# Kernel optimization log

Measured on AMD Instinct MI355X. Metric: run time of the kernel, lower is better.

The kernel has to match this reference:

```python
import jax, jax.numpy as jnp
import numpy as np

B, S, LATENT = 256, 64, 20
U_DIM = LATENT // 5            # 4
T_HID, T_DEPTH = 20, 4         # treatment MLP
D_HID, D_DEPTH = 4 * LATENT, 4 # drift MLP (80 hidden)
T_LEN = 41
DT = 0.05
SIGMA, THETA, MU = 0.5, 1.0, 0.0
N = B * S
DIM_AUG = LATENT + 2           # latent + logqp + Tx


def _mlp(x, w_in, b_in, w_h, b_h, w_out, b_out, act):
    # input layer always ReLU (MLPSimple), hidden layers use `act`
    h = jax.nn.relu(x @ w_in.T + b_in)
    for i in range(w_h.shape[0]):
        h = act(h @ w_h[i].T + b_h[i])
    return h @ w_out.T + b_out


def setup_inputs() -> dict:
    key = jax.random.key(0)
    ks = jax.random.split(key, 20)

    def lin(k, out_d, in_d):
        bound = 1.0 / np.sqrt(in_d)
        return jax.random.uniform(k, (out_d, in_d), jnp.float32, -bound, bound)

    def bias(k, out_d, in_d):
        bound = 1.0 / np.sqrt(in_d)
        return jax.random.uniform(k, (out_d,), jnp.float32, -bound, bound)

    return {
        "z_SDE": jax.random.normal(ks[0], (B, S, LATENT), jnp.float32),
        "t": jnp.arange(T_LEN, dtype=jnp.float32) * DT,
        "Tx": jax.random.uniform(ks[1], (B,), jnp.float32),
        "noise": jax.random.normal(ks[2], (T_LEN - 1, N, DIM_AUG), jnp.float32),
        # treatment MLP: 1 -> 20 (ReLU) -> [20->20 ReLU]x4 -> 4
        "tw_in": lin(ks[3], T_HID, 1),
        "tb_in": bias(ks[4], T_HID, 1),
        "tw_h": jnp.stack([lin(jax.random.fold_in(ks[5], i), T_HID, T_HID) for i in range(T_DEPTH)]),
        "tb_h": jnp.stack([bias(jax.random.fold_in(ks[6], i), T_HID, T_HID) for i in range(T_DEPTH)]),
        "tw_out": lin(ks[7], U_DIM, T_HID),
        "tb_out": bias(ks[8], U_DIM, T_HID),
        # drift MLP: 24 -> 80 (ReLU) -> [80->80 Tanh]x4 -> 20
        "dw_in": lin(ks[9], D_HID, LATENT + U_DIM),
        "db_in": bias(ks[10], D_HID, LATENT + U_DIM),
        "dw_h": jnp.stack([lin(jax.random.fold_in(ks[11], i), D_HID, D_HID) for i in range(D_DEPTH)]),
        "db_h": jnp.stack([bias(jax.random.fold_in(ks[12], i), D_HID, D_HID) for i in range(D_DEPTH)]),
        "dw_out": lin(ks[13], LATENT, D_HID),
        "db_out": bias(ks[14], LATENT, D_HID),
    }


def reference(z_SDE, t, Tx, noise, tw_in, tb_in, tw_h, tb_h, tw_out, tb_out,
              dw_in, db_in, dw_h, db_h, dw_out, db_out):
    # build augmented initial state: [z, logqp0=0, Tx]  -> [N, DIM_AUG]
    Tx_rep = jnp.broadcast_to(Tx[:, None, None], (B, S, 1))
    aug_y0 = jnp.concatenate(
        [z_SDE, jnp.zeros((B, S, 1), z_SDE.dtype), Tx_rep.astype(z_SDE.dtype)], axis=-1
    ).reshape(N, DIM_AUG)

    dt = t[1] - t[0]           # 0.05, aligned with euler dt
    sqrt_dt = jnp.sqrt(dt)
    # diagonal diffusion: sigma on latent dims, 0 on (logqp, Tx) aug dims
    g_diag = jnp.concatenate([jnp.full((LATENT,), SIGMA, jnp.float32), jnp.zeros((2,), jnp.float32)])

    def f_aug(ti, y_aug):
        T_ = y_aug[:, -1]                     # treatment indicator
        y = y_aug[:, :LATENT]
        t_col = jnp.broadcast_to(ti, (N, 1)).astype(y.dtype)
        u = _mlp(t_col, tw_in, tb_in, tw_h, tb_h, tw_out, tb_out, jax.nn.relu)
        u_t = u * T_[:, None]
        h = THETA * (MU - y)                  # prior drift
        f = _mlp(jnp.concatenate([y, u_t], axis=-1), dw_in, db_in, dw_h, db_h, dw_out, db_out, jnp.tanh) - h
        # _stable_division(f - h, g); g = sigma = 0.5 > eps so plain division
        uu = (f - h) / SIGMA
        f_logqp = 0.5 * jnp.sum(uu * uu, axis=1, keepdims=True)
        return jnp.concatenate([f, f_logqp, jnp.zeros_like(f_logqp)], axis=1)

    def step(y, inp):
        ti, dW = inp
        y_new = y + f_aug(ti, y) * dt + g_diag[None, :] * (dW * sqrt_dt)
        return y_new, y_new

    _, ys_rest = jax.lax.scan(step, aug_y0, (t[:-1], noise))
    aug_ys = jnp.concatenate([aug_y0[None], ys_rest], axis=0)   # [T, N, DIM_AUG]
    # faithful to source: raw reshape of [T, N, dim] into [B, S, T, dim]
    aug_ys = aug_ys.reshape(-1, S, T_LEN, DIM_AUG)
    ys = aug_ys[:, :, :, :-2]
    logqp = aug_ys[:, :, -1, -2]
    return ys, logqp
```

## Files before the change

kernel.cpp:

```cpp
#include <hip/hip_runtime.h>
#include <math.h>
#include <stdint.h>

#define NPART 16384
#define NSTEP 40
#define DIMA  22
#define OUT0_ELEMS 13434880
#define TRAJ_OFF   160

typedef __attribute__((ext_vector_type(8))) short short8;
typedef __attribute__((ext_vector_type(4))) float floatx4;
typedef __attribute__((ext_vector_type(4))) int   intx4;

union V4 { intx4 i; short8 s; floatx4 f; };

__device__ __forceinline__ uint32_t bf16r(float x) {
    uint32_t u = __float_as_uint(x);
    u += 0x7FFFu + ((u >> 16) & 1u);
    return u >> 16;
}
__device__ __forceinline__ uint32_t pk2(float a0, float a1) {
    return bf16r(a0) | (bf16r(a1) << 16);
}
__device__ __forceinline__ float fast_tanh(float x) {
    float e = __expf(2.0f * x);
    return 1.0f - 2.0f * __builtin_amdgcn_rcpf(e + 1.0f);
}

__device__ __forceinline__ V4 load8(const float* p) {
    floatx4 v0 = *(const floatx4*)p;
    floatx4 v1 = *(const floatx4*)(p + 4);
    V4 r;
    r.i = (intx4){ (int)pk2(v0[0], v0[1]), (int)pk2(v0[2], v0[3]),
                   (int)pk2(v1[0], v1[1]), (int)pk2(v1[2], v1[3]) };
    return r;
}

#define BUILD_B3(B0, B1, B2, PK)                                               \
    {                                                                          \
        _Pragma("unroll")                                                      \
        for (int w = 0; w < 4; w++) {                                          \
            int s = (((w >> 1) + 2 * quad) & 3) * 16 + n15;                    \
            int a0 = __shfl((int)PK[0][w & 1], s);                             \
            int a1 = __shfl((int)PK[1][w & 1], s);                             \
            B0[w] = (quad >= 2) ? a1 : a0;                                     \
            int a2 = __shfl((int)PK[2][w & 1], s);                             \
            int a3 = __shfl((int)PK[3][w & 1], s);                             \
            B1[w] = (quad >= 2) ? a3 : a2;                                     \
            int a4 = __shfl((int)PK[4][w & 1], s);                             \
            B2[w] = (quad >= 2) ? 0 : a4;                                      \
        }                                                                      \
    }

__global__ __launch_bounds__(256, 1) void sde_mfma(
    const float* __restrict__ z,      const float* __restrict__ t_arr,
    const float* __restrict__ Tx,     const float* __restrict__ noise,
    const float* __restrict__ dw_in,  const float* __restrict__ db_in,
    const float* __restrict__ dw_h,   const float* __restrict__ db_h,
    const float* __restrict__ dw_out, const float* __restrict__ db_out,
    const float* __restrict__ tw_in,  const float* __restrict__ tb_in,
    const float* __restrict__ tw_h,   const float* __restrict__ tb_h,
    const float* __restrict__ tw_out, const float* __restrict__ tb_out,
    float* __restrict__ out0,         float* __restrict__ traj)
{
    __shared__ float sb[592];
    const int tid = threadIdx.x;

    for (int di = tid; di < 432; di += 256) {
        float v;
        if (di < 80)       v = db_in[di];
        else if (di < 400) v = db_h[di - 80];
        else               v = (di - 400 < 20) ? db_out[di - 400] : 0.f;
        sb[di] = v;
    }
    if (tid < NSTEP) {
        float ti = t_arr[tid];
        float hh[20], h2[20];
        #pragma unroll
        for (int j = 0; j < 20; j++) {
            float v = tw_in[j] * ti + tb_in[j];
            hh[j] = v > 0.f ? v : 0.f;
        }
        #pragma unroll
        for (int l = 0; l < 4; l++) {
            #pragma unroll
            for (int j = 0; j < 20; j++) {
                float a = tb_h[l * 20 + j];
                #pragma unroll
                for (int k = 0; k < 20; k++) a += tw_h[(l * 20 + j) * 20 + k] * hh[k];
                h2[j] = a > 0.f ? a : 0.f;
            }
            #pragma unroll
            for (int j = 0; j < 20; j++) hh[j] = h2[j];
        }
        #pragma unroll
        for (int c = 0; c < 4; c++) {
            float a = tb_out[c];
            #pragma unroll
            for (int k = 0; k < 20; k++) a += tw_out[c * 20 + k] * hh[k];
            sb[432 + tid * 4 + c] = a;
        }
    }

    const int lane = tid & 63;
    const int n15  = lane & 15;
    const int quad = lane >> 4;
    const int wv   = tid >> 6;
    const int n    = blockIdx.x * 64 + wv * 16 + n15;
    const float Txb = Tx[blockIdx.x];
    const float dtv = t_arr[1] - t_arr[0];
    const float sdt = sqrtf(dtv);
    const intx4 zero4 = {0, 0, 0, 0};

    V4 wAin[5], wAh[4][5][3], wAout[2][3];
    {
        #pragma unroll
        for (int mt = 0; mt < 5; mt++) {
            if (quad < 3) wAin[mt] = load8(dw_in + (mt * 16 + n15) * 24 + quad * 8);
            else          wAin[mt].i = zero4;
        }
        #pragma unroll
        for (int l = 0; l < 4; l++)
            #pragma unroll
            for (int mt = 0; mt < 5; mt++) {
                const float* base = dw_h + l * 6400 + (mt * 16 + n15) * 80 + quad * 8;
                wAh[l][mt][0] = load8(base);
                wAh[l][mt][1] = load8(base + 32);
                if (quad < 2) wAh[l][mt][2] = load8(base + 64);
                else          wAh[l][mt][2].i = zero4;
            }
        #pragma unroll
        for (int mt = 0; mt < 2; mt++) {
            int m = mt * 16 + n15;
            bool mv = (m < 20);
            const float* base = dw_out + m * 80 + quad * 8;
            wAout[mt][0].i = mv ? load8(base).i      : zero4;
            wAout[mt][1].i = mv ? load8(base + 32).i : zero4;
            wAout[mt][2].i = (mv && quad < 2) ? load8(base + 64).i : zero4;
        }
    }
    __syncthreads();

    float y0[4], y1[4] = {0.f, 0.f, 0.f, 0.f};
    {
        floatx4 zv = *(const floatx4*)(z + (size_t)n * 20 + quad * 4);
        #pragma unroll
        for (int r = 0; r < 4; r++) y0[r] = zv[r];
        *(floatx4*)(out0 + (size_t)n * 20 + quad * 4) = zv;
        if (quad == 0) {
            floatx4 z2 = *(const floatx4*)(z + (size_t)n * 20 + 16);
            #pragma unroll
            for (int r = 0; r < 4; r++) y1[r] = z2[r];
            *(floatx4*)(out0 + (size_t)n * 20 + 16) = z2;
            traj[n] = 0.f;
        }
    }

    double lq = 0.0;
    for (int i = 0; i < NSTEP; i++) {
        size_t nbase = ((size_t)i * NPART + n) * DIMA;
        floatx4 dW0 = *(const floatx4*)(noise + nbase + quad * 4);
        floatx4 dW1 = {0.f, 0.f, 0.f, 0.f};
        if (quad == 0) dW1 = *(const floatx4*)(noise + nbase + 16);

        floatx4 uv = *(const floatx4*)(sb + 432 + i * 4);
        float ut0 = uv[0] * Txb, ut1 = uv[1] * Txb;
        float ut2 = uv[2] * Txb, ut3 = uv[3] * Txb;

        uint32_t p0[2] = { pk2(y0[0], y0[1]), pk2(y0[2], y0[3]) };
        uint32_t p1[2] = { 0, 0 };
        if (quad == 0)      { p1[0] = pk2(y1[0], y1[1]); p1[1] = pk2(y1[2], y1[3]); }
        else if (quad == 1) { p1[0] = pk2(ut0, ut1);     p1[1] = pk2(ut2, ut3); }
        V4 bin;
        #pragma unroll
        for (int w = 0; w < 4; w++) {
            int s = (((w >> 1) + 2 * quad) & 3) * 16 + n15;
            int lo = __shfl((int)p0[w & 1], s);
            int hi = __shfl((int)p1[w & 1], s);
            bin.i[w] = (quad >= 2) ? hi : lo;
        }

        floatx4 acc[5];
        #pragma unroll
        for (int mt = 0; mt < 5; mt++) {
            floatx4 c = *(const floatx4*)(sb + mt * 16 + quad * 4);
            acc[mt] = __builtin_amdgcn_mfma_f32_16x16x32_bf16(wAin[mt].s, bin.s, c, 0, 0, 0);
        }
        uint32_t pkA[5][2];
        #pragma unroll
        for (int mt = 0; mt < 5; mt++) {
            pkA[mt][0] = pk2(fmaxf(acc[mt][0], 0.f), fmaxf(acc[mt][1], 0.f));
            pkA[mt][1] = pk2(fmaxf(acc[mt][2], 0.f), fmaxf(acc[mt][3], 0.f));
        }

        #pragma unroll
        for (int l = 0; l < 4; l++) {
            int B0[4], B1[4], B2[4];
            BUILD_B3(B0, B1, B2, pkA);
            V4 b0, b1, b2;
            b0.i = (intx4){B0[0], B0[1], B0[2], B0[3]};
            b1.i = (intx4){B1[0], B1[1], B1[2], B1[3]};
            b2.i = (intx4){B2[0], B2[1], B2[2], B2[3]};
            #pragma unroll
            for (int mt = 0; mt < 5; mt++) {
                floatx4 c = *(const floatx4*)(sb + 80 + l * 80 + mt * 16 + quad * 4);
                c = __builtin_amdgcn_mfma_f32_16x16x32_bf16(wAh[l][mt][0].s, b0.s, c, 0, 0, 0);
                c = __builtin_amdgcn_mfma_f32_16x16x32_bf16(wAh[l][mt][1].s, b1.s, c, 0, 0, 0);
                c = __builtin_amdgcn_mfma_f32_16x16x32_bf16(wAh[l][mt][2].s, b2.s, c, 0, 0, 0);
                acc[mt] = c;
            }
            #pragma unroll
            for (int mt = 0; mt < 5; mt++) {
                pkA[mt][0] = pk2(fast_tanh(acc[mt][0]), fast_tanh(acc[mt][1]));
                pkA[mt][1] = pk2(fast_tanh(acc[mt][2]), fast_tanh(acc[mt][3]));
            }
        }

        int B0[4], B1[4], B2[4];
        BUILD_B3(B0, B1, B2, pkA);
        V4 b0, b1, b2;
        b0.i = (intx4){B0[0], B0[1], B0[2], B0[3]};
        b1.i = (intx4){B1[0], B1[1], B1[2], B1[3]};
        b2.i = (intx4){B2[0], B2[1], B2[2], B2[3]};
        floatx4 oacc[2];
        #pragma unroll
        for (int mt = 0; mt < 2; mt++) {
            floatx4 c = *(const floatx4*)(sb + 400 + mt * 16 + quad * 4);
            c = __builtin_amdgcn_mfma_f32_16x16x32_bf16(wAout[mt][0].s, b0.s, c, 0, 0, 0);
            c = __builtin_amdgcn_mfma_f32_16x16x32_bf16(wAout[mt][1].s, b1.s, c, 0, 0, 0);
            oacc[mt] = __builtin_amdgcn_mfma_f32_16x16x32_bf16(wAout[mt][2].s, b2.s, c, 0, 0, 0);
        }

        float part = 0.f;
        size_t obase = ((size_t)(i + 1) * NPART + n) * 20;
        floatx4 st;
        #pragma unroll
        for (int r = 0; r < 4; r++) {
            float o = oacc[0][r];
            float y = y0[r];
            float f = o + y;
            float uu = 2.f * o + 4.f * y;
            part += uu * uu;
            y0[r] = y + f * dtv + (0.5f * sdt) * dW0[r];
            st[r] = y0[r];
        }
        *(floatx4*)(out0 + obase + quad * 4) = st;
        if (quad == 0) {
            floatx4 st2;
            #pragma unroll
            for (int r = 0; r < 4; r++) {
                float o = oacc[1][r];
                float y = y1[r];
                float f = o + y;
                float uu = 2.f * o + 4.f * y;
                part += uu * uu;
                y1[r] = y + f * dtv + (0.5f * sdt) * dW1[r];
                st2[r] = y1[r];
            }
            *(floatx4*)(out0 + obase + 16) = st2;
        }
        part += __shfl_xor(part, 16);
        part += __shfl_xor(part, 32);
        lq += 0.5 * (double)part * (double)dtv;
        if (quad == 0) traj[(size_t)(i + 1) * NPART + n] = (float)lq;
    }
}

__global__ void gather_logqp(const float* __restrict__ traj, float* __restrict__ out1) {
    int i = blockIdx.x * 256 + threadIdx.x;
    if (i < NPART) out1[i] = traj[(size_t)41 * i + 40];
}

extern "C" void kernel_launch(void* const* d_in, const int* in_sizes, int n_in,
                              void* d_out, int out_size, void* d_ws, size_t ws_size,
                              hipStream_t stream) {
    const float* z      = (const float*)d_in[0];
    const float* t_arr  = (const float*)d_in[1];
    const float* Tx     = (const float*)d_in[2];
    const float* noise  = (const float*)d_in[3];
    const float* tw_in  = (const float*)d_in[4];
    const float* tb_in  = (const float*)d_in[5];
    const float* tw_h   = (const float*)d_in[6];
    const float* tb_h   = (const float*)d_in[7];
    const float* tw_out = (const float*)d_in[8];
    const float* tb_out = (const float*)d_in[9];
    const float* dw_in  = (const float*)d_in[10];
    const float* db_in  = (const float*)d_in[11];
    const float* dw_h   = (const float*)d_in[12];
    const float* db_h   = (const float*)d_in[13];
    const float* dw_out = (const float*)d_in[14];
    const float* db_out = (const float*)d_in[15];

    float* wsf  = (float*)d_ws;
    float* traj = wsf + TRAJ_OFF;
    float* out0 = (float*)d_out;
    float* out1 = out0 + OUT0_ELEMS;

    hipLaunchKernelGGL(sde_mfma, dim3(256), dim3(256), 0, stream,
                       z, t_arr, Tx, noise, dw_in, db_in, dw_h, db_h,
                       dw_out, db_out, tw_in, tb_in, tw_h, tb_h, tw_out, tb_out,
                       out0, traj);
    hipLaunchKernelGGL(gather_logqp, dim3(64), dim3(256), 0, stream, traj, out1);
}
```

Baseline: 310.9 us.

## Stage permuted bf16 weights in LDS and drop cross-lane shuffles

Weights are no longer held in registers. They are pre-packed into LDS as bf16 in a permuted K ordering that matches the MFMA output layout, so activations can feed the next layer's B operand directly with no __shfl rebuilding. Biases move from LDS into registers. This removes many shuffles per layer and frees a large block of VGPRs, at the cost of LDS reads of A fragments on every step and a more complex staging prologue.

```diff
diff --git a/kernel.cpp b/kernel.cpp
--- a/kernel.cpp
+++ b/kernel.cpp
@@ -11,8 +11,16 @@
 typedef __attribute__((ext_vector_type(8))) short short8;
 typedef __attribute__((ext_vector_type(4))) float floatx4;
 typedef __attribute__((ext_vector_type(4))) int   intx4;
+typedef __attribute__((ext_vector_type(2))) int   intx2;
 
 union V4 { intx4 i; short8 s; floatx4 f; };
+
+#define AIN_B   0
+#define AH_B    5120
+#define AOUT_B  56320
+#define U_B     61440
+#define LDS_BYTES 62080
+#define STAGE_DW  15360
 
 __device__ __forceinline__ uint32_t bf16r(float x) {
     uint32_t u = __float_as_uint(x);
@@ -26,31 +34,6 @@
     float e = __expf(2.0f * x);
     return 1.0f - 2.0f * __builtin_amdgcn_rcpf(e + 1.0f);
 }
-
-__device__ __forceinline__ V4 load8(const float* p) {
-    floatx4 v0 = *(const floatx4*)p;
-    floatx4 v1 = *(const floatx4*)(p + 4);
-    V4 r;
-    r.i = (intx4){ (int)pk2(v0[0], v0[1]), (int)pk2(v0[2], v0[3]),
-                   (int)pk2(v1[0], v1[1]), (int)pk2(v1[2], v1[3]) };
-    return r;
-}
-
-#define BUILD_B3(B0, B1, B2, PK)                                               \
-    {                                                                          \
-        _Pragma("unroll")                                                      \
-        for (int w = 0; w < 4; w++) {                                          \
-            int s = (((w >> 1) + 2 * quad) & 3) * 16 + n15;                    \
-            int a0 = __shfl((int)PK[0][w & 1], s);                             \
-            int a1 = __shfl((int)PK[1][w & 1], s);                             \
-            B0[w] = (quad >= 2) ? a1 : a0;                                     \
-            int a2 = __shfl((int)PK[2][w & 1], s);                             \
-            int a3 = __shfl((int)PK[3][w & 1], s);                             \
-            B1[w] = (quad >= 2) ? a3 : a2;                                     \
-            int a4 = __shfl((int)PK[4][w & 1], s);                             \
-            B2[w] = (quad >= 2) ? 0 : a4;                                      \
-        }                                                                      \
-    }
 
 __global__ __launch_bounds__(256, 1) void sde_mfma(
     const float* __restrict__ z,      const float* __restrict__ t_arr,
@@ -63,15 +46,52 @@
     const float* __restrict__ tw_out, const float* __restrict__ tb_out,
     float* __restrict__ out0,         float* __restrict__ traj)
 {
-    __shared__ float sb[592];
+    __shared__ __align__(16) uint8_t lds[LDS_BYTES];
     const int tid = threadIdx.x;
 
-    for (int di = tid; di < 432; di += 256) {
-        float v;
-        if (di < 80)       v = db_in[di];
-        else if (di < 400) v = db_h[di - 80];
-        else               v = (di - 400 < 20) ? db_out[di - 400] : 0.f;
-        sb[di] = v;
+    for (int di = tid; di < STAGE_DW; di += 256) {
+        uint32_t val = 0u;
+        if (di < 1280) {
+            int r = di & 255, lane = r >> 2, w = r & 3;
+            int m = lane & 15, q = lane >> 4, mt = di >> 8;
+            int f = -1;
+            if (w < 2)            f = 4 * q + 2 * w;
+            else if (q == 0)      f = 16 + 2 * (w - 2);
+            else if (q == 1)      f = 20 + 2 * (w - 2);
+            if (f >= 0) val = pk2(dw_in[(mt * 16 + m) * 24 + f],
+                                  dw_in[(mt * 16 + m) * 24 + f + 1]);
+        } else if (di < 14080) {
+            int q2 = di - 1280, g = q2 / 640, r = q2 % 640;
+            int l = g / 5, mt = g % 5;
+            int lane, f;
+            if (r < 512) {
+                int kt = r >> 8, rr = r & 255, w = rr & 3;
+                lane = rr >> 2;
+                f = 16 * (2 * kt + (w >> 1)) + 4 * (lane >> 4) + 2 * (w & 1);
+            } else {
+                int rr = r - 512, d = rr & 1;
+                lane = rr >> 1;
+                f = 64 + 4 * (lane >> 4) + 2 * d;
+            }
+            int m = lane & 15;
+            val = pk2(dw_h[l * 6400 + (mt * 16 + m) * 80 + f],
+                      dw_h[l * 6400 + (mt * 16 + m) * 80 + f + 1]);
+        } else {
+            int q2 = di - 14080, mt = q2 / 640, r = q2 % 640;
+            int lane, f;
+            if (r < 512) {
+                int kt = r >> 8, rr = r & 255, w = rr & 3;
+                lane = rr >> 2;
+                f = 16 * (2 * kt + (w >> 1)) + 4 * (lane >> 4) + 2 * (w & 1);
+            } else {
+                int rr = r - 512, d = rr & 1;
+                lane = rr >> 1;
+                f = 64 + 4 * (lane >> 4) + 2 * d;
+            }
+            int m = mt * 16 + (lane & 15);
+            if (m < 20) val = pk2(dw_out[m * 80 + f], dw_out[m * 80 + f + 1]);
+        }
+        ((uint32_t*)lds)[di] = val;
     }
     if (tid < NSTEP) {
         float ti = t_arr[tid];
@@ -98,7 +118,7 @@
             float a = tb_out[c];
             #pragma unroll
             for (int k = 0; k < 20; k++) a += tw_out[c * 20 + k] * hh[k];
-            sb[432 + tid * 4 + c] = a;
+            ((float*)(lds + U_B))[tid * 4 + c] = a;
         }
     }
 
@@ -110,35 +130,19 @@
     const float Txb = Tx[blockIdx.x];
     const float dtv = t_arr[1] - t_arr[0];
     const float sdt = sqrtf(dtv);
-    const intx4 zero4 = {0, 0, 0, 0};
-
-    V4 wAin[5], wAh[4][5][3], wAout[2][3];
-    {
-        #pragma unroll
-        for (int mt = 0; mt < 5; mt++) {
-            if (quad < 3) wAin[mt] = load8(dw_in + (mt * 16 + n15) * 24 + quad * 8);
-            else          wAin[mt].i = zero4;
-        }
-        #pragma unroll
-        for (int l = 0; l < 4; l++)
-            #pragma unroll
-            for (int mt = 0; mt < 5; mt++) {
-                const float* base = dw_h + l * 6400 + (mt * 16 + n15) * 80 + quad * 8;
-                wAh[l][mt][0] = load8(base);
-                wAh[l][mt][1] = load8(base + 32);
-                if (quad < 2) wAh[l][mt][2] = load8(base + 64);
-                else          wAh[l][mt][2].i = zero4;
-            }
-        #pragma unroll
-        for (int mt = 0; mt < 2; mt++) {
-            int m = mt * 16 + n15;
-            bool mv = (m < 20);
-            const float* base = dw_out + m * 80 + quad * 8;
-            wAout[mt][0].i = mv ? load8(base).i      : zero4;
-            wAout[mt][1].i = mv ? load8(base + 32).i : zero4;
-            wAout[mt][2].i = (mv && quad < 2) ? load8(base + 64).i : zero4;
-        }
-    }
+
+    floatx4 cIn[5], cH[4][5], cOut[2];
+    #pragma unroll
+    for (int mt = 0; mt < 5; mt++)
+        cIn[mt] = *(const floatx4*)(db_in + mt * 16 + quad * 4);
+    #pragma unroll
+    for (int l = 0; l < 4; l++)
+        #pragma unroll
+        for (int mt = 0; mt < 5; mt++)
+            cH[l][mt] = *(const floatx4*)(db_h + l * 80 + mt * 16 + quad * 4);
+    cOut[0] = *(const floatx4*)(db_out + quad * 4);
+    cOut[1] = (quad == 0) ? *(const floatx4*)(db_out + 16)
+                          : (floatx4){0.f, 0.f, 0.f, 0.f};
     __syncthreads();
 
     float y0[4], y1[4] = {0.f, 0.f, 0.f, 0.f};
@@ -163,28 +167,22 @@
         floatx4 dW1 = {0.f, 0.f, 0.f, 0.f};
         if (quad == 0) dW1 = *(const floatx4*)(noise + nbase + 16);
 
-        floatx4 uv = *(const floatx4*)(sb + 432 + i * 4);
-        float ut0 = uv[0] * Txb, ut1 = uv[1] * Txb;
-        float ut2 = uv[2] * Txb, ut3 = uv[3] * Txb;
-
-        uint32_t p0[2] = { pk2(y0[0], y0[1]), pk2(y0[2], y0[3]) };
-        uint32_t p1[2] = { 0, 0 };
-        if (quad == 0)      { p1[0] = pk2(y1[0], y1[1]); p1[1] = pk2(y1[2], y1[3]); }
-        else if (quad == 1) { p1[0] = pk2(ut0, ut1);     p1[1] = pk2(ut2, ut3); }
+        const float* su = (const float*)(lds + U_B) + i * 4;
+        float ut0 = su[0] * Txb, ut1 = su[1] * Txb;
+        float ut2 = su[2] * Txb, ut3 = su[3] * Txb;
+
         V4 bin;
-        #pragma unroll
-        for (int w = 0; w < 4; w++) {
-            int s = (((w >> 1) + 2 * quad) & 3) * 16 + n15;
-            int lo = __shfl((int)p0[w & 1], s);
-            int hi = __shfl((int)p1[w & 1], s);
-            bin.i[w] = (quad >= 2) ? hi : lo;
-        }
+        bin.i[0] = pk2(y0[0], y0[1]);
+        bin.i[1] = pk2(y0[2], y0[3]);
+        if (quad == 0)      { bin.i[2] = pk2(y1[0], y1[1]); bin.i[3] = pk2(y1[2], y1[3]); }
+        else if (quad == 1) { bin.i[2] = pk2(ut0, ut1);     bin.i[3] = pk2(ut2, ut3); }
+        else                { bin.i[2] = 0;                 bin.i[3] = 0; }
 
         floatx4 acc[5];
         #pragma unroll
         for (int mt = 0; mt < 5; mt++) {
-            floatx4 c = *(const floatx4*)(sb + mt * 16 + quad * 4);
-            acc[mt] = __builtin_amdgcn_mfma_f32_16x16x32_bf16(wAin[mt].s, bin.s, c, 0, 0, 0);
+            V4 a; a.i = *(const intx4*)(lds + AIN_B + mt * 1024 + lane * 16);
+            acc[mt] = __builtin_amdgcn_mfma_f32_16x16x32_bf16(a.s, bin.s, cIn[mt], 0, 0, 0);
         }
         uint32_t pkA[5][2];
         #pragma unroll
@@ -195,18 +193,21 @@
 
         #pragma unroll
         for (int l = 0; l < 4; l++) {
-            int B0[4], B1[4], B2[4];
-            BUILD_B3(B0, B1, B2, pkA);
             V4 b0, b1, b2;
-            b0.i = (intx4){B0[0], B0[1], B0[2], B0[3]};
-            b1.i = (intx4){B1[0], B1[1], B1[2], B1[3]};
-            b2.i = (intx4){B2[0], B2[1], B2[2], B2[3]};
+            b0.i = (intx4){(int)pkA[0][0], (int)pkA[0][1], (int)pkA[1][0], (int)pkA[1][1]};
+            b1.i = (intx4){(int)pkA[2][0], (int)pkA[2][1], (int)pkA[3][0], (int)pkA[3][1]};
+            b2.i = (intx4){(int)pkA[4][0], (int)pkA[4][1], 0, 0};
             #pragma unroll
             for (int mt = 0; mt < 5; mt++) {
-                floatx4 c = *(const floatx4*)(sb + 80 + l * 80 + mt * 16 + quad * 4);
-                c = __builtin_amdgcn_mfma_f32_16x16x32_bf16(wAh[l][mt][0].s, b0.s, c, 0, 0, 0);
-                c = __builtin_amdgcn_mfma_f32_16x16x32_bf16(wAh[l][mt][1].s, b1.s, c, 0, 0, 0);
-                c = __builtin_amdgcn_mfma_f32_16x16x32_bf16(wAh[l][mt][2].s, b2.s, c, 0, 0, 0);
+                const uint8_t* grp = lds + AH_B + (size_t)(l * 5 + mt) * 2560;
+                V4 a0; a0.i = *(const intx4*)(grp + lane * 16);
+                V4 a1; a1.i = *(const intx4*)(grp + 1024 + lane * 16);
+                intx2 h2 = *(const intx2*)(grp + 2048 + lane * 8);
+                V4 a2; a2.i = (intx4){h2[0], h2[1], 0, 0};
+                floatx4 c = cH[l][mt];
+                c = __builtin_amdgcn_mfma_f32_16x16x32_bf16(a0.s, b0.s, c, 0, 0, 0);
+                c = __builtin_amdgcn_mfma_f32_16x16x32_bf16(a1.s, b1.s, c, 0, 0, 0);
+                c = __builtin_amdgcn_mfma_f32_16x16x32_bf16(a2.s, b2.s, c, 0, 0, 0);
                 acc[mt] = c;
             }
             #pragma unroll
@@ -216,19 +217,22 @@
             }
         }
 
-        int B0[4], B1[4], B2[4];
-        BUILD_B3(B0, B1, B2, pkA);
         V4 b0, b1, b2;
-        b0.i = (intx4){B0[0], B0[1], B0[2], B0[3]};
-        b1.i = (intx4){B1[0], B1[1], B1[2], B1[3]};
-        b2.i = (intx4){B2[0], B2[1], B2[2], B2[3]};
+        b0.i = (intx4){(int)pkA[0][0], (int)pkA[0][1], (int)pkA[1][0], (int)pkA[1][1]};
+        b1.i = (intx4){(int)pkA[2][0], (int)pkA[2][1], (int)pkA[3][0], (int)pkA[3][1]};
+        b2.i = (intx4){(int)pkA[4][0], (int)pkA[4][1], 0, 0};
         floatx4 oacc[2];
         #pragma unroll
         for (int mt = 0; mt < 2; mt++) {
-            floatx4 c = *(const floatx4*)(sb + 400 + mt * 16 + quad * 4);
-            c = __builtin_amdgcn_mfma_f32_16x16x32_bf16(wAout[mt][0].s, b0.s, c, 0, 0, 0);
-            c = __builtin_amdgcn_mfma_f32_16x16x32_bf16(wAout[mt][1].s, b1.s, c, 0, 0, 0);
-            oacc[mt] = __builtin_amdgcn_mfma_f32_16x16x32_bf16(wAout[mt][2].s, b2.s, c, 0, 0, 0);
+            const uint8_t* grp = lds + AOUT_B + (size_t)mt * 2560;
+            V4 a0; a0.i = *(const intx4*)(grp + lane * 16);
+            V4 a1; a1.i = *(const intx4*)(grp + 1024 + lane * 16);
+            intx2 h2 = *(const intx2*)(grp + 2048 + lane * 8);
+            V4 a2; a2.i = (intx4){h2[0], h2[1], 0, 0};
+            floatx4 c = cOut[mt];
+            c = __builtin_amdgcn_mfma_f32_16x16x32_bf16(a0.s, b0.s, c, 0, 0, 0);
+            c = __builtin_amdgcn_mfma_f32_16x16x32_bf16(a1.s, b1.s, c, 0, 0, 0);
+            oacc[mt] = __builtin_amdgcn_mfma_f32_16x16x32_bf16(a2.s, b2.s, c, 0, 0, 0);
         }
 
         float part = 0.f;
```

Result: faster. 274.8 us (-11.6%).
